# Performance work log

Hardware: AMD Instinct MI355X
Metric: run time of the kernel (lower is better)

Reference implementation:

```python
import jax, jax.numpy as jnp
import numpy as np

EMBED = 1024
HEADS = 16
HEAD_DIM = EMBED // HEADS
LN_EPS = 1e-5


def setup_inputs() -> dict:
    key = jax.random.key(0)
    ks = jax.random.split(key, 12)
    B, LQ, LK = 2, 2048, 2048
    s = 1.0 / np.sqrt(EMBED)
    inp = {
        "query_seq": jax.random.normal(ks[0], (B, LQ, EMBED), jnp.float32),
        "key_value_seq": jax.random.normal(ks[1], (B, LK, EMBED), jnp.float32),
        "prompt_size": 0,
        "Wq": jax.random.normal(ks[2], (EMBED, EMBED), jnp.float32) * s,
        "bq": jnp.zeros((EMBED,), jnp.float32),
        "Wk": jax.random.normal(ks[3], (EMBED, EMBED), jnp.float32) * s,
        "bk": jnp.zeros((EMBED,), jnp.float32),
        "Wv": jax.random.normal(ks[4], (EMBED, EMBED), jnp.float32) * s,
        "bv": jnp.zeros((EMBED,), jnp.float32),
        "Wo": jax.random.normal(ks[5], (EMBED, EMBED), jnp.float32) * s,
        "bo": jnp.zeros((EMBED,), jnp.float32),
        "ln_gamma": jnp.ones((EMBED,), jnp.float32),
        "ln_beta": jnp.zeros((EMBED,), jnp.float32),
    }
    return inp


def _split_heads(x):
    B, L, _ = x.shape
    return x.reshape(B, L, HEADS, HEAD_DIM).transpose(0, 2, 1, 3)  # [B,H,L,Dh]


def reference(query_seq, key_value_seq, prompt_size, Wq, bq, Wk, bk, Wv, bv, Wo, bo, ln_gamma, ln_beta):
    # projections (torch nn.Linear: x @ W.T + b)
    q = _split_heads(query_seq @ Wq.T + bq)
    k = _split_heads(key_value_seq @ Wk.T + bk)
    v = _split_heads(key_value_seq @ Wv.T + bv)
    # naive attention: full score matrix, softmax over keys
    scores = jnp.einsum("bhqd,bhkd->bhqk", q, k) / np.sqrt(HEAD_DIM).astype(np.float32)
    attn = jax.nn.softmax(scores, axis=-1)
    ctx = jnp.einsum("bhqk,bhkd->bhqd", attn, v)
    B, H, LQ, Dh = ctx.shape
    ctx = ctx.transpose(0, 2, 1, 3).reshape(B, LQ, H * Dh)
    out = ctx @ Wo.T + bo
    # residual + LayerNorm
    x = out + query_seq
    mu = jnp.mean(x, axis=-1, keepdims=True)
    var = jnp.var(x, axis=-1, keepdims=True)
    return (x - mu) * jax.lax.rsqrt(var + LN_EPS) * ln_gamma + ln_beta
```

## Files before the change

### kernel.cpp

```cpp
#include <hip/hip_runtime.h>

typedef unsigned short u16;
typedef unsigned int u32;
typedef __attribute__((ext_vector_type(8))) __bf16 bf16x8;
typedef __attribute__((ext_vector_type(4))) float f32x4;
typedef __attribute__((ext_vector_type(16))) float f32x16;

#define EMBED 1024
#define NB 2
#define LQ 2048
#define HEADS 16
#define DH 64
#define QSCALE 0.18033688011112042f

__device__ __forceinline__ u16 f2bf(float f) {
  u32 u = __float_as_uint(f);
  u32 r = (u + 0x7FFFu + ((u >> 16) & 1u)) >> 16;
  return (u16)r;
}

__device__ __forceinline__ void glds16(const void* g, void* l) {
  __builtin_amdgcn_global_load_lds((const __attribute__((address_space(1))) void*)g,
                                   (__attribute__((address_space(3))) void*)l, 16, 0, 0);
}

__device__ __forceinline__ f32x4 mfma16(bf16x8 a, bf16x8 b, f32x4 c) {
  return __builtin_amdgcn_mfma_f32_16x16x32_bf16(a, b, c, 0, 0, 0);
}
__device__ __forceinline__ f32x16 mfma32(bf16x8 a, bf16x8 b, f32x16 c) {
  return __builtin_amdgcn_mfma_f32_32x32x16_bf16(a, b, c, 0, 0, 0);
}

__device__ __forceinline__ void pl32(u32& a, u32& b) {
  asm("v_permlane32_swap_b32 %0, %1" : "+v"(a), "+v"(b));
}

__device__ __forceinline__ u32 packbf(float a, float b) {
  return __builtin_amdgcn_perm(__float_as_uint(b), __float_as_uint(a), 0x07060302u);
}

__global__ __launch_bounds__(256) void cast_kernel(
    const float* __restrict__ q, const float* __restrict__ kv,
    const float* __restrict__ wq, const float* __restrict__ wk,
    const float* __restrict__ wv, const float* __restrict__ wo,
    u16* __restrict__ qb, u16* __restrict__ kvb, u16* __restrict__ wqb,
    u16* __restrict__ wkb, u16* __restrict__ wvb, u16* __restrict__ wob) {
  int bid = blockIdx.x;
  const float* src;
  u16* dst;
  long base;
  if (bid < 2048) {
    src = q; dst = qb; base = (long)bid * 2048;
  } else if (bid < 4096) {
    src = kv; dst = kvb; base = (long)(bid - 2048) * 2048;
  } else {
    int wsel = (bid - 4096) >> 9;
    int wb = (bid - 4096) & 511;
    if (wsel == 0) { src = wq; dst = wqb; }
    else if (wsel == 1) { src = wk; dst = wkb; }
    else if (wsel == 2) { src = wv; dst = wvb; }
    else { src = wo; dst = wob; }
    base = (long)wb * 2048;
  }
  long e = base + (long)threadIdx.x * 8;
  float4 f0 = *(const float4*)(src + e);
  float4 f1 = *(const float4*)(src + e + 4);
  uint4 o;
  o.x = (u32)f2bf(f0.x) | ((u32)f2bf(f0.y) << 16);
  o.y = (u32)f2bf(f0.z) | ((u32)f2bf(f0.w) << 16);
  o.z = (u32)f2bf(f1.x) | ((u32)f2bf(f1.y) << 16);
  o.w = (u32)f2bf(f1.z) | ((u32)f2bf(f1.w) << 16);
  *(uint4*)(dst + e) = o;
}

template <int IT>
__device__ __forceinline__ void gemm_core(
    u16* As, u16* Bs, const u16* __restrict__ A, const u16* __restrict__ W,
    const float* __restrict__ bias, const float* __restrict__ resid,
    void* __restrict__ outp, int mode, int bx, int by) {
  const int K = EMBED;
  const int TM = IT * 32;
  const int tid = threadIdx.x;
  const int lane = tid & 63;
  const int wv = tid >> 6;
  const int wm = wv >> 1, wn = wv & 1;
  const int l16 = lane & 15, quad = lane >> 4;
  const long tile_m = (long)bx * TM;
  const long tile_n = (long)by * 128;

  f32x4 z4 = {0.f, 0.f, 0.f, 0.f};
  f32x4 acc[IT][4];
#pragma unroll
  for (int i = 0; i < IT; i++)
#pragma unroll
    for (int j = 0; j < 4; j++) acc[i][j] = z4;

  for (int k0 = 0; k0 < K; k0 += 64) {
#pragma unroll
    for (int it = 0; it < TM / 32; it++) {
      int lin = it * 256 + tid;
      int row = lin >> 3, cc = lin & 7;
      glds16(A + (tile_m + row) * K + k0 + ((cc ^ (row & 7)) << 3), As + lin * 8);
    }
#pragma unroll
    for (int it = 0; it < 4; it++) {
      int lin = it * 256 + tid;
      int row = lin >> 3, cc = lin & 7;
      glds16(W + (tile_n + row) * K + k0 + ((cc ^ (row & 7)) << 3), Bs + lin * 8);
    }
    __syncthreads();
#pragma unroll
    for (int ki = 0; ki < 2; ki++) {
      bf16x8 af[IT], bfr[4];
#pragma unroll
      for (int i = 0; i < IT; i++) {
        int row = wm * (IT * 16) + i * 16 + l16;
        af[i] = *(const bf16x8*)(As + row * 64 + (((ki * 4 + quad) ^ (row & 7)) << 3));
      }
#pragma unroll
      for (int j = 0; j < 4; j++) {
        int row = wn * 64 + j * 16 + l16;
        bfr[j] = *(const bf16x8*)(Bs + row * 64 + (((ki * 4 + quad) ^ (row & 7)) << 3));
      }
#pragma unroll
      for (int i = 0; i < IT; i++)
#pragma unroll
        for (int j = 0; j < 4; j++) acc[i][j] = mfma16(af[i], bfr[j], acc[i][j]);
    }
    __syncthreads();
  }

#pragma unroll
  for (int j = 0; j < 4; j++) {
    int gn = (int)tile_n + wn * 64 + j * 16 + l16;
    float bv = bias[gn];
#pragma unroll
    for (int i = 0; i < IT; i++) {
      long gm0 = tile_m + wm * (IT * 16) + i * 16 + quad * 4;
      if (mode == 3) {
#pragma unroll
        for (int r = 0; r < 4; r++) {
          long idx = (gm0 + r) * EMBED + gn;
          ((float*)outp)[idx] = acc[i][j][r] + bv + resid[idx];
        }
      } else if (mode == 2) {
        int b = (int)(gm0 >> 11), l = (int)(gm0 & 2047);
        int hh = gn >> 6, dh = gn & 63;
        uint2 pk;
        pk.x = (u32)f2bf(acc[i][j][0] + bv) | ((u32)f2bf(acc[i][j][1] + bv) << 16);
        pk.y = (u32)f2bf(acc[i][j][2] + bv) | ((u32)f2bf(acc[i][j][3] + bv) << 16);
        *(uint2*)((u16*)outp + (long)((b * HEADS + hh) * DH + dh) * LQ + l) = pk;
      } else {
#pragma unroll
        for (int r = 0; r < 4; r++) {
          long gm = gm0 + r;
          float v = acc[i][j][r] + bv;
          if (mode == 0) v *= QSCALE;
          int b = (int)(gm >> 11), l = (int)(gm & 2047);
          int hh = gn >> 6, dh = gn & 63;
          ((u16*)outp)[(long)((b * HEADS + hh) * LQ + l) * DH + dh] = f2bf(v);
        }
      }
    }
  }
}

__global__ __launch_bounds__(256, 4) void qkv_kernel(
    const u16* __restrict__ qb, const u16* __restrict__ kvb,
    const u16* __restrict__ wqb, const u16* __restrict__ wkb, const u16* __restrict__ wvb,
    const float* __restrict__ bq, const float* __restrict__ bk, const float* __restrict__ bv,
    u16* __restrict__ Qh, u16* __restrict__ Kh, u16* __restrict__ Vt) {
  __shared__ u16 As[64 * 64];
  __shared__ u16 Bs[128 * 64];
  if (blockIdx.z == 0)      gemm_core<2>(As, Bs, qb,  wqb, bq, nullptr, Qh, 0, blockIdx.x, blockIdx.y);
  else if (blockIdx.z == 1) gemm_core<2>(As, Bs, kvb, wkb, bk, nullptr, Kh, 1, blockIdx.x, blockIdx.y);
  else                      gemm_core<2>(As, Bs, kvb, wvb, bv, nullptr, Vt, 2, blockIdx.x, blockIdx.y);
}

__global__ __launch_bounds__(256, 4) void oproj_kernel(
    const u16* __restrict__ ctx, const u16* __restrict__ wob,
    const float* __restrict__ bo, const float* __restrict__ resid, float* __restrict__ out) {
  __shared__ u16 As[64 * 64];
  __shared__ u16 Bs[128 * 64];
  gemm_core<2>(As, Bs, ctx, wob, bo, resid, out, 3, blockIdx.x, blockIdx.y);
}

__global__ __launch_bounds__(256, 2) void attn_kernel(
    const u16* __restrict__ Qh, const u16* __restrict__ Kh,
    const u16* __restrict__ Vt, u16* __restrict__ ctx) {
  __shared__ u16 Qs[128 * 64];
  __shared__ u16 KVs[3][2][64 * 64];
  const int tid = threadIdx.x;
  const int lane = tid & 63;
  const int wv = tid >> 6;
  const int l32 = lane & 31, h = lane >> 5;
  const int qt = blockIdx.x, bh = blockIdx.y;
  const long qoff = (long)bh * (LQ * DH) + (long)qt * (128 * DH);
  const long koff = (long)bh * (LQ * DH);
  const long voff = (long)bh * (DH * LQ);
  const int qbase = wv * 32;

#define STAGE_KV(t, N)                                                          \
  do {                                                                          \
    _Pragma("unroll") for (int it = 0; it < 2; it++) {                          \
      int lin = it * 256 + tid;                                                 \
      int row = lin >> 3, cc = lin & 7;                                         \
      glds16(Kh + koff + (long)((t) * 64 + row) * 64 + ((cc ^ (row & 7)) << 3), \
             &KVs[N][0][0] + lin * 8);                                          \
      glds16(Vt + voff + (long)row * LQ + (t) * 64 + ((cc ^ (row & 7)) << 3),   \
             &KVs[N][1][0] + lin * 8);                                          \
    }                                                                           \
  } while (0)

#pragma unroll
  for (int it = 0; it < 4; it++) {
    int lin = it * 256 + tid;
    int row = lin >> 3, cc = lin & 7;
    glds16(Qh + qoff + row * 64 + ((cc ^ (row & 7)) << 3), Qs + lin * 8);
  }
  STAGE_KV(0, 0);
  STAGE_KV(1, 1);
  __syncthreads();

  bf16x8 bq[4];
  {
    int row = qbase + l32;
#pragma unroll
    for (int ks = 0; ks < 4; ks++)
      bq[ks] = *(const bf16x8*)(Qs + row * 64 + (((ks * 2 + h) ^ (row & 7)) << 3));
  }

  f32x16 z16 = {0.f, 0.f, 0.f, 0.f, 0.f, 0.f, 0.f, 0.f,
                0.f, 0.f, 0.f, 0.f, 0.f, 0.f, 0.f, 0.f};
  f32x16 ot[2];
  ot[0] = z16;
  ot[1] = z16;
  f32x16 sta[2], stb[2];
  uint2 pk[2][4];
  float2 ls2 = {0.f, 0.f};

#define DO_S(C, ST)                                                              \
  do {                                                                           \
    __builtin_amdgcn_s_setprio(1);                                               \
    _Pragma("unroll") for (int ks = 0; ks < 4; ks++) {                           \
      _Pragma("unroll") for (int mt = 0; mt < 2; mt++) {                         \
        int row = mt * 32 + l32;                                                 \
        bf16x8 ak = *(const bf16x8*)(&KVs[C][0][0] + row * 64 +                  \
                                     (((ks * 2 + h) ^ (row & 7)) << 3));         \
        ST[mt] = mfma32(ak, bq[ks], (ks == 0) ? z16 : ST[mt]);                   \
      }                                                                          \
    }                                                                            \
    __builtin_amdgcn_s_setprio(0);                                               \
  } while (0)

#define DO_SM(ST)                                                                \
  do {                                                                           \
    _Pragma("unroll") for (int mt = 0; mt < 2; mt++) {                           \
      _Pragma("unroll") for (int g = 0; g < 4; g++) {                            \
        float p0 = __builtin_amdgcn_exp2f(ST[mt][g * 4 + 0]);                    \
        float p1 = __builtin_amdgcn_exp2f(ST[mt][g * 4 + 1]);                    \
        float p2 = __builtin_amdgcn_exp2f(ST[mt][g * 4 + 2]);                    \
        float p3 = __builtin_amdgcn_exp2f(ST[mt][g * 4 + 3]);                    \
        ls2.x += p0 + p2;                                                        \
        ls2.y += p1 + p3;                                                        \
        pk[mt][g].x = packbf(p0, p1);                                            \
        pk[mt][g].y = packbf(p2, p3);                                            \
      }                                                                          \
    }                                                                            \
  } while (0)

#define DO_PV(P)                                                                 \
  do {                                                                           \
    _Pragma("unroll") for (int s = 0; s < 4; s++) {                              \
      uint2 wa = pk[s >> 1][(s & 1) * 2];                                        \
      uint2 wb = pk[s >> 1][(s & 1) * 2 + 1];                                    \
      u32 a0 = wa.x, b0 = wb.x, a1 = wa.y, b1 = wb.y;                            \
      pl32(a0, b0);                                                              \
      pl32(a1, b1);                                                              \
      union { u32 u[4]; bf16x8 v; } bp;                                          \
      bp.u[0] = a0;                                                              \
      bp.u[1] = a1;                                                              \
      bp.u[2] = b0;                                                              \
      bp.u[3] = b1;                                                              \
      __builtin_amdgcn_s_setprio(1);                                             \
      _Pragma("unroll") for (int mt2 = 0; mt2 < 2; mt2++) {                      \
        int row = mt2 * 32 + l32;                                                \
        bf16x8 av = *(const bf16x8*)(&KVs[P][1][0] + row * 64 +                  \
                                     ((((s << 1) + h) ^ (row & 7)) << 3));       \
        ot[mt2] = mfma32(av, bp.v, ot[mt2]);                                     \
      }                                                                          \
      __builtin_amdgcn_s_setprio(0);                                             \
    }                                                                            \
  } while (0)

#define AITER(kt, P, C, N, STW, STR)                                             \
  do {                                                                           \
    if ((kt) + 1 < 32) STAGE_KV((kt) + 1, N);                                    \
    DO_S(C, STW);                                                                \
    DO_SM(STR);                                                                  \
    DO_PV(P);                                                                    \
    __syncthreads();                                                             \
  } while (0)

  DO_S(0, sta);

  AITER(1, 0, 1, 2, stb, sta);
  for (int k0 = 2; k0 < 32; k0 += 6) {
    AITER(k0 + 0, 1, 2, 0, sta, stb);
    AITER(k0 + 1, 2, 0, 1, stb, sta);
    AITER(k0 + 2, 0, 1, 2, sta, stb);
    AITER(k0 + 3, 1, 2, 0, stb, sta);
    AITER(k0 + 4, 2, 0, 1, sta, stb);
    AITER(k0 + 5, 0, 1, 2, stb, sta);
  }
  DO_SM(stb);
  DO_PV(1);

#undef STAGE_KV
#undef DO_S
#undef DO_SM
#undef DO_PV
#undef AITER

  float lsum = ls2.x + ls2.y;
  lsum += __shfl_xor(lsum, 32);
  float inv = 1.0f / lsum;

  const int b = bh >> 4, head = bh & 15;
  int qrow = qt * 128 + qbase + l32;
  long base = (long)(b * LQ + qrow) * EMBED + head * DH;
#pragma unroll
  for (int mt = 0; mt < 2; mt++) {
#pragma unroll
    for (int g = 0; g < 4; g++) {
      uint2 pkk;
      pkk.x = (u32)f2bf(ot[mt][g * 4 + 0] * inv) | ((u32)f2bf(ot[mt][g * 4 + 1] * inv) << 16);
      pkk.y = (u32)f2bf(ot[mt][g * 4 + 2] * inv) | ((u32)f2bf(ot[mt][g * 4 + 3] * inv) << 16);
      *(uint2*)(ctx + base + mt * 32 + g * 8 + 4 * h) = pkk;
    }
  }
}

__global__ __launch_bounds__(256) void ln_kernel(
    float* __restrict__ x, const float* __restrict__ gamma, const float* __restrict__ beta) {
  __shared__ float red[8];
  const int tid = threadIdx.x;
  const long row = blockIdx.x;
  float4 v = *(const float4*)(x + row * EMBED + tid * 4);
  float s = v.x + v.y + v.z + v.w;
  float sq = v.x * v.x + v.y * v.y + v.z * v.z + v.w * v.w;
#pragma unroll
  for (int off = 1; off < 64; off <<= 1) {
    s += __shfl_xor(s, off);
    sq += __shfl_xor(sq, off);
  }
  if ((tid & 63) == 0) {
    red[(tid >> 6) * 2] = s;
    red[(tid >> 6) * 2 + 1] = sq;
  }
  __syncthreads();
  s = red[0] + red[2] + red[4] + red[6];
  sq = red[1] + red[3] + red[5] + red[7];
  float mu = s * (1.f / EMBED);
  float var = sq * (1.f / EMBED) - mu * mu;
  float rstd = rsqrtf(var + 1e-5f);
  float4 g = *(const float4*)(gamma + tid * 4);
  float4 bt = *(const float4*)(beta + tid * 4);
  float4 ov;
  ov.x = (v.x - mu) * rstd * g.x + bt.x;
  ov.y = (v.y - mu) * rstd * g.y + bt.y;
  ov.z = (v.z - mu) * rstd * g.z + bt.z;
  ov.w = (v.w - mu) * rstd * g.w + bt.w;
  *(float4*)(x + row * EMBED + tid * 4) = ov;
}

extern "C" void kernel_launch(void* const* d_in, const int* in_sizes, int n_in,
                              void* d_out, int out_size, void* d_ws, size_t ws_size,
                              hipStream_t stream) {
  const float* q     = (const float*)d_in[0];
  const float* kv    = (const float*)d_in[1];
  const float* Wq    = (const float*)d_in[3];
  const float* bq    = (const float*)d_in[4];
  const float* Wk    = (const float*)d_in[5];
  const float* bk    = (const float*)d_in[6];
  const float* Wv    = (const float*)d_in[7];
  const float* bv    = (const float*)d_in[8];
  const float* Wo    = (const float*)d_in[9];
  const float* bo    = (const float*)d_in[10];
  const float* gamma = (const float*)d_in[11];
  const float* beta  = (const float*)d_in[12];

  char* ws = (char*)d_ws;
  u16* qb  = (u16*)(ws + (0l  << 20));
  u16* kvb = (u16*)(ws + (8l  << 20));
  u16* wqb = (u16*)(ws + (16l << 20));
  u16* wkb = (u16*)(ws + (18l << 20));
  u16* wvb = (u16*)(ws + (20l << 20));
  u16* wob = (u16*)(ws + (22l << 20));
  u16* Qh  = (u16*)(ws + (24l << 20));
  u16* Kh  = (u16*)(ws + (32l << 20));
  u16* Vt  = (u16*)(ws + (40l << 20));
  u16* ctx = (u16*)(ws + (48l << 20));
  float* out = (float*)d_out;

  cast_kernel<<<6144, 256, 0, stream>>>(q, kv, Wq, Wk, Wv, Wo, qb, kvb, wqb, wkb, wvb, wob);
  qkv_kernel<<<dim3(64, 8, 3), 256, 0, stream>>>(qb, kvb, wqb, wkb, wvb, bq, bk, bv, Qh, Kh, Vt);
  attn_kernel<<<dim3(16, 32), 256, 0, stream>>>(Qh, Kh, Vt, ctx);
  oproj_kernel<<<dim3(64, 8), 256, 0, stream>>>(ctx, wob, bo, q, out);
  ln_kernel<<<4096, 256, 0, stream>>>(out, gamma, beta);
}
```

Before: 247.7 us.

## Deepen attention KV pipeline to four buffers with vmcnt-based partial waits

The attention kernel now loads Q fragments straight from global memory into registers, which drops the Q shared-memory staging and frees LDS for a fourth K/V buffer. K/V tiles are prefetched two iterations ahead. Each full __syncthreads is replaced by an s_waitcnt vmcnt(N) plus a barrier, so only the older loads must finish before the barrier. The score tile uses a single register set, with softmax of the previous tile issued before the next S matmul. This is meant to hide global-load latency better, at the cost of more LDS per block, which may reduce occupancy, and a more fragile hand-tuned wait count.

Measured after the change: 207.7 us. 16.1% less time.

```diff
diff --git a/kernel.cpp b/kernel.cpp
--- a/kernel.cpp
+++ b/kernel.cpp
@@ -188,8 +188,7 @@
 __global__ __launch_bounds__(256, 2) void attn_kernel(
     const u16* __restrict__ Qh, const u16* __restrict__ Kh,
     const u16* __restrict__ Vt, u16* __restrict__ ctx) {
-  __shared__ u16 Qs[128 * 64];
-  __shared__ u16 KVs[3][2][64 * 64];
+  __shared__ u16 KVs[4][2][64 * 64];
   const int tid = threadIdx.x;
   const int lane = tid & 63;
   const int wv = tid >> 6;
@@ -212,34 +211,35 @@
     }                                                                           \
   } while (0)
 
-#pragma unroll
-  for (int it = 0; it < 4; it++) {
-    int lin = it * 256 + tid;
-    int row = lin >> 3, cc = lin & 7;
-    glds16(Qh + qoff + row * 64 + ((cc ^ (row & 7)) << 3), Qs + lin * 8);
-  }
+#define SYNC(W)                                                                 \
+  do {                                                                          \
+    asm volatile("s_waitcnt vmcnt(" #W ")" ::: "memory");                       \
+    __builtin_amdgcn_s_barrier();                                               \
+    asm volatile("" ::: "memory");                                              \
+  } while (0)
+
+  bf16x8 bq[4];
+  {
+    const u16* qp = Qh + qoff + (qbase + l32) * 64 + h * 8;
+#pragma unroll
+    for (int ks = 0; ks < 4; ks++) bq[ks] = *(const bf16x8*)(qp + ks * 16);
+  }
+
   STAGE_KV(0, 0);
   STAGE_KV(1, 1);
-  __syncthreads();
-
-  bf16x8 bq[4];
-  {
-    int row = qbase + l32;
-#pragma unroll
-    for (int ks = 0; ks < 4; ks++)
-      bq[ks] = *(const bf16x8*)(Qs + row * 64 + (((ks * 2 + h) ^ (row & 7)) << 3));
-  }
+  STAGE_KV(2, 2);
+  SYNC(4);
 
   f32x16 z16 = {0.f, 0.f, 0.f, 0.f, 0.f, 0.f, 0.f, 0.f,
                 0.f, 0.f, 0.f, 0.f, 0.f, 0.f, 0.f, 0.f};
   f32x16 ot[2];
   ot[0] = z16;
   ot[1] = z16;
-  f32x16 sta[2], stb[2];
+  f32x16 st[2];
   uint2 pk[2][4];
   float2 ls2 = {0.f, 0.f};
 
-#define DO_S(C, ST)                                                              \
+#define DO_S(C)                                                                  \
   do {                                                                           \
     __builtin_amdgcn_s_setprio(1);                                               \
     _Pragma("unroll") for (int ks = 0; ks < 4; ks++) {                           \
@@ -247,20 +247,20 @@
         int row = mt * 32 + l32;                                                 \
         bf16x8 ak = *(const bf16x8*)(&KVs[C][0][0] + row * 64 +                  \
                                      (((ks * 2 + h) ^ (row & 7)) << 3));         \
-        ST[mt] = mfma32(ak, bq[ks], (ks == 0) ? z16 : ST[mt]);                   \
+        st[mt] = mfma32(ak, bq[ks], (ks == 0) ? z16 : st[mt]);                   \
       }                                                                          \
     }                                                                            \
     __builtin_amdgcn_s_setprio(0);                                               \
   } while (0)
 
-#define DO_SM(ST)                                                                \
+#define DO_SM()                                                                  \
   do {                                                                           \
     _Pragma("unroll") for (int mt = 0; mt < 2; mt++) {                           \
       _Pragma("unroll") for (int g = 0; g < 4; g++) {                            \
-        float p0 = __builtin_amdgcn_exp2f(ST[mt][g * 4 + 0]);                    \
-        float p1 = __builtin_amdgcn_exp2f(ST[mt][g * 4 + 1]);                    \
-        float p2 = __builtin_amdgcn_exp2f(ST[mt][g * 4 + 2]);                    \
-        float p3 = __builtin_amdgcn_exp2f(ST[mt][g * 4 + 3]);                    \
+        float p0 = __builtin_amdgcn_exp2f(st[mt][g * 4 + 0]);                    \
+        float p1 = __builtin_amdgcn_exp2f(st[mt][g * 4 + 1]);                    \
+        float p2 = __builtin_amdgcn_exp2f(st[mt][g * 4 + 2]);                    \
+        float p3 = __builtin_amdgcn_exp2f(st[mt][g * 4 + 3]);                    \
         ls2.x += p0 + p2;                                                        \
         ls2.y += p1 + p3;                                                        \
         pk[mt][g].x = packbf(p0, p1);                                            \
@@ -293,30 +293,31 @@
     }                                                                            \
   } while (0)
 
-#define AITER(kt, P, C, N, STW, STR)                                             \
+#define AITER(kt, P, C, N, W)                                                    \
   do {                                                                           \
-    if ((kt) + 1 < 32) STAGE_KV((kt) + 1, N);                                    \
-    DO_S(C, STW);                                                                \
-    DO_SM(STR);                                                                  \
+    if ((kt) + 2 < 32) STAGE_KV((kt) + 2, N);                                    \
+    DO_SM();                                                                     \
+    DO_S(C);                                                                     \
     DO_PV(P);                                                                    \
-    __syncthreads();                                                             \
-  } while (0)
-
-  DO_S(0, sta);
-
-  AITER(1, 0, 1, 2, stb, sta);
-  for (int k0 = 2; k0 < 32; k0 += 6) {
-    AITER(k0 + 0, 1, 2, 0, sta, stb);
-    AITER(k0 + 1, 2, 0, 1, stb, sta);
-    AITER(k0 + 2, 0, 1, 2, sta, stb);
-    AITER(k0 + 3, 1, 2, 0, stb, sta);
-    AITER(k0 + 4, 2, 0, 1, sta, stb);
-    AITER(k0 + 5, 0, 1, 2, stb, sta);
-  }
-  DO_SM(stb);
-  DO_PV(1);
+    SYNC(W);                                                                     \
+  } while (0)
+
+  DO_S(0);
+
+  AITER(1, 0, 1, 3, 4);
+  for (int k0 = 2; k0 < 30; k0 += 4) {
+    AITER(k0 + 0, 1, 2, 0, 4);
+    AITER(k0 + 1, 2, 3, 1, 4);
+    AITER(k0 + 2, 3, 0, 2, 4);
+    AITER(k0 + 3, 0, 1, 3, 4);
+  }
+  AITER(30, 1, 2, 0, 0);
+  AITER(31, 2, 3, 1, 0);
+  DO_SM();
+  DO_PV(3);
 
 #undef STAGE_KV
+#undef SYNC
 #undef DO_S
 #undef DO_SM
 #undef DO_PV
```
